# Kernel tuning notes

Measured on AMD Instinct MI355X. Metric: run time of the kernel, lower is better.

The kernel has to match this reference:

```python
import jax, jax.numpy as jnp
import numpy as np
from jax import lax

B, S, N, FD = 4, 12, 307, 3
E = 64; F = 64; H = 64; K = 3; HEADS = 4; P = 12; DFF = 64


def setup_inputs() -> dict:
    key = jax.random.key(0)
    ks = jax.random.split(key, 24)
    rn = lambda i, shape, s=0.1: jax.random.normal(ks[i], shape, dtype=jnp.float32) * s
    z = lambda n: jnp.zeros((n,), jnp.float32)
    return {
        'x': jax.random.normal(ks[0], (B, S, N, FD), dtype=jnp.float32),
        'cheb': rn(1, (K, N, N), 0.05),
        'theta': rn(2, (K, E, F)),
        'W_emb_x': rn(3, (1, E)), 'b_emb_x': z(E),
        'W_emb_os': rn(4, (FD - 1, E)), 'b_emb_os': z(E),
        'U_x': rn(5, (F, 4 * H)), 'V_x': rn(6, (H, 4 * H)), 'b_x': z(4 * H),
        'U_g': rn(7, (F, 2 * H)), 'V_g': rn(8, (H, 2 * H)), 'b_g': z(2 * H),
        'W_ff1': rn(9, (H, DFF)), 'b_ff1': z(DFF), 'W_ff2': rn(10, (DFF, H)), 'b_ff2': z(H),
        'W_tc': rn(11, (F, H, 1, 3)), 'b_tc': z(F),
        'W_rc': rn(12, (F, H, 1, 1)), 'b_rc': z(F),
        'W_in': rn(13, (3 * F, F)), 'b_in': z(3 * F),
        'W_out': rn(14, (F, F)), 'b_out': z(F),
        'W_fa1': rn(15, (F, DFF)), 'b_fa1': z(DFF), 'W_fa2': rn(16, (DFF, F)), 'b_fa2': z(F),
        'W_fin': rn(17, (P, S, 1, F)), 'b_fin': z(P),
    }


def _forward(x, cheb, theta, W_emb_x, b_emb_x, W_emb_os, b_emb_os,
             U_x, V_x, b_x, U_g, V_g, b_g, W_ff1, b_ff1, W_ff2, b_ff2,
             W_tc, b_tc, W_rc, b_rc, W_in, b_in, W_out, b_out,
             W_fa1, b_fa1, W_fa2, b_fa2, W_fin, b_fin):
    # token embeddings (dropout=0 -> identity)
    emb_x = x[..., :1] @ W_emb_x + b_emb_x          # (B,S,N,E)
    emb_os = x[..., 1:] @ W_emb_os + b_emb_os       # (B,S,N,E)

    def cheb_conv(h):
        # sum_k relu-after-sum of T_k @ h @ theta_k
        agg = jnp.einsum('kmn,bsnc->kbsmc', cheb, h)
        return jax.nn.relu(jnp.einsum('kbsmc,kcd->bsmd', agg, theta))

    gcn_x = cheb_conv(emb_x)                        # (B,S,N,F)
    gcn_os = cheb_conv(emb_os)                      # (B,S,N,F)

    # Glstm: precompute input projections, scan the recurrence over time
    gx = jnp.einsum('bsnc,cf->sbnf', gcn_x, U_x) + b_x    # (S,B,N,4H)
    gg = jnp.einsum('bsnc,cf->sbnf', gcn_os, U_g) + b_g   # (S,B,N,2H)

    h0 = jnp.zeros((B, N, H), x.dtype)
    c0 = jnp.zeros((B, N, H), x.dtype)

    def step(carry, inp):
        ht, ct = carry
        gx_t, gg_t = inp
        gates = jax.nn.sigmoid(gx_t + ht @ V_x)     # ft,it,ot,ut all sigmoid (as in source)
        gov = jax.nn.sigmoid(gg_t + ht @ V_g)
        ft, it, ot, ut = jnp.split(gates, 4, axis=-1)
        gf, gu = jnp.split(gov, 2, axis=-1)
        ct = gf * ft * ct + gu * it * ut
        ht = ot * jnp.tanh(ct)
        return (ht, ct), ht

    _, hs = lax.scan(step, (h0, c0), (gx, gg))
    hidden = jnp.moveaxis(hs, 0, 1)                 # (B,S,N,H)
    # Muti_glstm output feedforward
    hidden = jax.nn.relu(hidden @ W_ff1 + b_ff1) @ W_ff2 + b_ff2

    # time conv: (1,3) kernel over time axis, pad 1
    hs_nchw = jnp.transpose(hidden, (0, 3, 2, 1))   # (B,H,N,S)
    tc = lax.conv_general_dilated(hs_nchw, W_tc, (1, 1), ((0, 0), (1, 1)),
                                  dimension_numbers=('NCHW', 'OIHW', 'NCHW'))
    tc = jnp.transpose(tc + b_tc[None, :, None, None], (0, 3, 2, 1))  # (B,S,N,F)

    # query = last time step, repeated over S
    query = jnp.broadcast_to(tc[:, -1:], (B, S, N, F))
    q_in = jnp.reshape(jnp.swapaxes(query, 2, 3), (B * N, S, F))
    kv_in = jnp.reshape(jnp.swapaxes(emb_x, 2, 3), (B * N, S, E))

    # torch MHA (batch_first=False): seq axis is dim0 (L=B*N), batch axis is dim1 (S)
    hd = F // HEADS
    Wq, Wk, Wv = jnp.split(W_in, 3, axis=0)
    bq, bk, bv = jnp.split(b_in, 3)

    def proj(t, Wp, bp):
        L = t.shape[0]
        p = t @ Wp.T + bp                            # (L, S, F)
        return jnp.transpose(p.reshape(L, S * HEADS, hd), (1, 0, 2))  # (S*HEADS, L, hd)

    qh = proj(q_in, Wq, bq)
    kh = proj(kv_in, Wk, bk)
    vh = proj(kv_in, Wv, bv)
    scores = jnp.einsum('hld,hmd->hlm', qh, kh) / np.float32(np.sqrt(hd))
    attn = jax.nn.softmax(scores, axis=-1)
    ctx = jnp.einsum('hlm,hmd->hld', attn, vh)       # (S*HEADS, B*N, hd)
    ctx = jnp.transpose(ctx, (1, 0, 2)).reshape(B * N, S, F)
    dsa = ctx @ W_out.T + b_out                      # (B*N, S, F)

    dsa = jnp.swapaxes(dsa.reshape(B, N, S, F), 1, 2)  # (B,S,N,F)
    ffa = jax.nn.relu(dsa @ W_fa1 + b_fa1) @ W_fa2 + b_fa2
    # residual 1x1 conv over channels of hidden
    res = jnp.einsum('bsnh,fh->bsnf', hidden, W_rc[:, :, 0, 0]) + b_rc
    comb = res + ffa                                 # (B,S,N,F)
    # final conv: channels=S, kernel (1,F) valid, then take last width index
    out = jnp.einsum('bsnf,psf->bpn', comb, W_fin[:, :, 0, :]) + b_fin[None, :, None]
    return out                                       # (B, pre_len, N)


def reference(x, cheb, theta, W_emb_x, b_emb_x, W_emb_os, b_emb_os,
              U_x, V_x, b_x, U_g, V_g, b_g, W_ff1, b_ff1, W_ff2, b_ff2,
              W_tc, b_tc, W_rc, b_rc, W_in, b_in, W_out, b_out,
              W_fa1, b_fa1, W_fa2, b_fa2, W_fin, b_fin):
    return _forward(x, cheb, theta, W_emb_x, b_emb_x, W_emb_os, b_emb_os,
                    U_x, V_x, b_x, U_g, V_g, b_g, W_ff1, b_ff1, W_ff2, b_ff2,
                    W_tc, b_tc, W_rc, b_rc, W_in, b_in, W_out, b_out,
                    W_fa1, b_fa1, W_fa2, b_fa2, W_fin, b_fin)
```

## Files before the change

kernel.cpp:

```cpp
#include <hip/hip_runtime.h>
#include <hip/hip_bf16.h>

#define BB 4
#define SS 12
#define NN 307
#define LL 1228
#define BSC 48
#define GG 48
#define WS_CX    0
#define WS_CROW  132624
#define WS_TXD   133568
#define WS_TBD   133760
#define WS_T1D   133952
#define WS_T2D   134144
#define WS_TOB   134336
#define WS_WRCT  134528
#define WS_WOT   138624
#define WS_H2    142720
#define WS_TFL   1085824
#define WS_XFL   1164416
#define WS_QH    2107520
#define WS_KH    3050624
#define WS_VH    3993728
#define WS_CTX   4936832

__global__ __launch_bounds__(256) void k1_precomp(
    const float* __restrict__ theta, const float* __restrict__ Wex,
    const float* __restrict__ bex, const float* __restrict__ Weos,
    const float* __restrict__ beos, const float* __restrict__ W_rc,
    const float* __restrict__ W_out, float* __restrict__ ws) {
  int tid = threadIdx.x;
  if (tid < 192) {
    int k = tid / 64, d = tid % 64;
    float a0 = 0.f, a1 = 0.f, a2 = 0.f, a3 = 0.f, a4 = 0.f;
    for (int c = 0; c < 64; ++c) {
      float th = theta[(k * 64 + c) * 64 + d];
      a0 = fmaf(Wex[c], th, a0);
      a1 = fmaf(bex[c], th, a1);
      a2 = fmaf(Weos[c], th, a2);
      a3 = fmaf(Weos[64 + c], th, a3);
      a4 = fmaf(beos[c], th, a4);
    }
    ws[WS_TXD + tid] = a0; ws[WS_TBD + tid] = a1; ws[WS_T1D + tid] = a2;
    ws[WS_T2D + tid] = a3; ws[WS_TOB + tid] = a4;
  }
  for (int i = tid; i < 4096; i += 256) {
    int hh = i >> 6, f = i & 63;
    ws[WS_WRCT + i] = W_rc[f * 64 + hh];
    ws[WS_WOT + i]  = W_out[f * 64 + hh];
  }
}

__global__ __launch_bounds__(320) void k2_cx(const float* __restrict__ x,
                                             const float* __restrict__ cheb,
                                             float* __restrict__ ws) {
  int k = blockIdx.x / BSC, bs = blockIdx.x % BSC;
  __shared__ float xl[921];
  for (int i = threadIdx.x; i < 921; i += 320) xl[i] = x[bs * 921 + i];
  __syncthreads();
  int m = threadIdx.x;
  if (m < NN) {
    const float* ch = cheb + (k * NN + m) * NN;
    float a0 = 0.f, a1 = 0.f, a2 = 0.f, ar = 0.f;
    for (int n = 0; n < NN; ++n) {
      float c = ch[n];
      ar += c;
      a0 = fmaf(c, xl[3 * n], a0);
      a1 = fmaf(c, xl[3 * n + 1], a1);
      a2 = fmaf(c, xl[3 * n + 2], a2);
    }
    ws[WS_CX + ((k * 3 + 0) * BSC + bs) * NN + m] = a0;
    ws[WS_CX + ((k * 3 + 1) * BSC + bs) * NN + m] = a1;
    ws[WS_CX + ((k * 3 + 2) * BSC + bs) * NN + m] = a2;
    if (bs == 0) ws[WS_CROW + k * NN + m] = ar;
  }
}

__global__ __launch_bounds__(256) void k2c_xfl(const float* __restrict__ x,
                                               const float* __restrict__ Wex,
                                               const float* __restrict__ bex,
                                               float* __restrict__ ws) {
  int idx = blockIdx.x * 256 + threadIdx.x;
  if (idx < 943104) {
    int n = idx % NN;
    int t = idx / NN;
    int e = t & 63;
    int bs = t >> 6;
    ws[WS_XFL + idx] = fmaf(x[(bs * NN + n) * 3], Wex[e], bex[e]);
  }
}

__global__ __launch_bounds__(384) void k3_scan(
    const float* __restrict__ U_x, const float* __restrict__ V_x,
    const float* __restrict__ b_x, const float* __restrict__ U_g,
    const float* __restrict__ V_g, const float* __restrict__ b_g,
    const float* __restrict__ W_ff1, const float* __restrict__ b_ff1,
    const float* __restrict__ W_ff2, const float* __restrict__ b_ff2,
    const float* __restrict__ W_tc, const float* __restrict__ b_tc,
    float* __restrict__ ws) {
  int l = blockIdx.x;
  int b = l / NN, n = l % NN;
  int tid = threadIdx.x;
  __shared__ float gcx[768], gcos[768], hsb[768], sg[256], sv[128];

  for (int idx = tid; idx < 768; idx += 384) {
    int s = idx >> 6, d = idx & 63;
    int bs = b * SS + s;
    float ax = 0.f, ao = 0.f;
#pragma unroll
    for (int k = 0; k < 3; ++k) {
      float c0 = ws[WS_CX + ((k * 3 + 0) * BSC + bs) * NN + n];
      float c1 = ws[WS_CX + ((k * 3 + 1) * BSC + bs) * NN + n];
      float c2 = ws[WS_CX + ((k * 3 + 2) * BSC + bs) * NN + n];
      float cr = ws[WS_CROW + k * NN + n];
      ax += c0 * ws[WS_TXD + k * 64 + d] + cr * ws[WS_TBD + k * 64 + d];
      ao += c1 * ws[WS_T1D + k * 64 + d] + c2 * ws[WS_T2D + k * 64 + d] +
            cr * ws[WS_TOB + k * 64 + d];
    }
    gcx[idx] = fmaxf(ax, 0.f);
    gcos[idx] = fmaxf(ao, 0.f);
  }
  __syncthreads();

  float gr[12];
  float vcol[64];
  if (tid < 256) {
#pragma unroll
    for (int s = 0; s < 12; ++s) gr[s] = b_x[tid];
    for (int c = 0; c < 64; ++c) {
      float u = U_x[c * 256 + tid];
#pragma unroll
      for (int s = 0; s < 12; ++s) gr[s] = fmaf(gcx[s * 64 + c], u, gr[s]);
    }
#pragma unroll
    for (int c = 0; c < 64; ++c) vcol[c] = V_x[c * 256 + tid];
  } else {
    int j = tid - 256;
#pragma unroll
    for (int s = 0; s < 12; ++s) gr[s] = b_g[j];
    for (int c = 0; c < 64; ++c) {
      float u = U_g[c * 128 + j];
#pragma unroll
      for (int s = 0; s < 12; ++s) gr[s] = fmaf(gcos[s * 64 + c], u, gr[s]);
    }
#pragma unroll
    for (int c = 0; c < 64; ++c) vcol[c] = V_g[c * 128 + j];
  }

  float ct = 0.f;
  for (int s = 0; s < 12; ++s) {
    float a = gr[s];
    if (s > 0) {
      const float* hp = &hsb[(s - 1) * 64];
#pragma unroll
      for (int h = 0; h < 64; ++h) a = fmaf(hp[h], vcol[h], a);
    }
    float sig = 1.f / (1.f + __expf(-a));
    if (tid < 256) sg[tid] = sig; else sv[tid - 256] = sig;
    __syncthreads();
    if (tid < 64) {
      ct = sv[tid] * sg[tid] * ct + sv[64 + tid] * sg[64 + tid] * sg[192 + tid];
      hsb[s * 64 + tid] = sg[128 + tid] * tanhf(ct);
    }
    __syncthreads();
  }

  for (int idx = tid; idx < 768; idx += 384) {
    int s = idx >> 6, d = idx & 63;
    float a = b_ff1[d];
    for (int c = 0; c < 64; ++c) a = fmaf(hsb[s * 64 + c], W_ff1[c * 64 + d], a);
    gcx[idx] = fmaxf(a, 0.f);
  }
  __syncthreads();
  for (int idx = tid; idx < 768; idx += 384) {
    int s = idx >> 6, h = idx & 63;
    float a = b_ff2[h];
    for (int d = 0; d < 64; ++d) a = fmaf(gcx[s * 64 + d], W_ff2[d * 64 + h], a);
    ws[WS_H2 + ((b * SS + s) * NN + n) * 64 + h] = a;
    gcos[idx] = a;
  }
  __syncthreads();
  if (tid < 64) {
    int f = tid;
    float a = b_tc[f];
    for (int h = 0; h < 64; ++h) {
      a = fmaf(gcos[10 * 64 + h], W_tc[(f * 64 + h) * 3 + 0], a);
      a = fmaf(gcos[11 * 64 + h], W_tc[(f * 64 + h) * 3 + 1], a);
    }
    ws[WS_TFL + (b * 64 + f) * NN + n] = a;
  }
}

__global__ __launch_bounds__(256) void k5_qkv(const float* __restrict__ W_in,
                                              const float* __restrict__ b_in,
                                              float* __restrict__ ws) {
  int blk = blockIdx.x;
  int g = blk / 77, mt = blk % 77;
  int s = g >> 2, a = g & 3;
  int m0 = mt * 16;
  __shared__ float xw[16][64], qw[16][64];
  for (int i = threadIdx.x; i < 1024; i += 256) {
    int mi = i >> 6, e = i & 63;
    int m = m0 + mi;
    if (m < LL) {
      int base = m * 768 + s * 64;
      xw[mi][e] = ws[WS_XFL + base + e];
      int bq = base / 235776;
      int off = base % 19648;
      qw[mi][e] = ws[WS_TFL + bq * 19648 + off + e];
    }
  }
  __syncthreads();
  int mi = threadIdx.x >> 4, d = threadIdx.x & 15;
  int m = m0 + mi;
  if (m < LL) {
    int f = a * 16 + d;
    float aq = b_in[f], ak = b_in[64 + f], av = b_in[128 + f];
    for (int e = 0; e < 64; ++e) {
      aq = fmaf(qw[mi][e], W_in[f * 64 + e], aq);
      ak = fmaf(xw[mi][e], W_in[(64 + f) * 64 + e], ak);
      av = fmaf(xw[mi][e], W_in[(128 + f) * 64 + e], av);
    }
    int o = (g * LL + m) * 16 + d;
    ws[WS_QH + o] = aq; ws[WS_KH + o] = ak; ws[WS_VH + o] = av;
  }
}

__global__ __launch_bounds__(512) void k6_attn(float* __restrict__ ws) {
  int blk = blockIdx.x;
  int g = blk / 20, qt = blk % 20;
  int s = g >> 2, a = g & 3;
  int tid = threadIdx.x;
  int w = tid >> 6;
  int qi = tid & 63;
  int l = qt * 64 + qi;
  bool act = (l < LL);

  __shared__ float sh[9728];
  float* kt = sh;
  float* vt = sh + 4096;

  float q[16];
  if (act) {
    const float4* qp = reinterpret_cast<const float4*>(ws + WS_QH + (g * LL + l) * 16);
#pragma unroll
    for (int jj = 0; jj < 4; ++jj) {
      float4 t = qp[jj];
      q[4 * jj + 0] = t.x * 0.25f; q[4 * jj + 1] = t.y * 0.25f;
      q[4 * jj + 2] = t.z * 0.25f; q[4 * jj + 3] = t.w * 0.25f;
    }
  } else {
#pragma unroll
    for (int d = 0; d < 16; ++d) q[d] = 0.f;
  }
  float cx[16];
#pragma unroll
  for (int d = 0; d < 16; ++d) cx[d] = 0.f;
  float mx = -1e30f, den = 0.f;

  const float4* kb = reinterpret_cast<const float4*>(ws + WS_KH + g * LL * 16);
  const float4* vb = reinterpret_cast<const float4*>(ws + WS_VH + g * LL * 16);
  float4* kt4 = reinterpret_cast<float4*>(kt);
  float4* vt4 = reinterpret_cast<float4*>(vt);

  for (int mt = 0; mt < 5; ++mt) {
    int mbase = mt * 256;
    int cnt = LL - mbase; if (cnt > 256) cnt = 256;
    int nf4 = cnt * 4;
    for (int i = tid; i < nf4; i += 512) {
      kt4[i] = kb[mbase * 4 + i];
      vt4[i] = vb[mbase * 4 + i];
    }
    __syncthreads();
    int e0 = w * 32;
    int e1 = e0 + 32; if (e1 > cnt) e1 = cnt;
    for (int mi = e0; mi < e1; ++mi) {
      const float4* kp = kt4 + mi * 4;
      float4 ka = kp[0], kb4 = kp[1], kc = kp[2], kd = kp[3];
      float p = q[0] * ka.x;
      p = fmaf(q[1], ka.y, p);  p = fmaf(q[2], ka.z, p);  p = fmaf(q[3], ka.w, p);
      p = fmaf(q[4], kb4.x, p); p = fmaf(q[5], kb4.y, p); p = fmaf(q[6], kb4.z, p);
      p = fmaf(q[7], kb4.w, p); p = fmaf(q[8], kc.x, p);  p = fmaf(q[9], kc.y, p);
      p = fmaf(q[10], kc.z, p); p = fmaf(q[11], kc.w, p); p = fmaf(q[12], kd.x, p);
      p = fmaf(q[13], kd.y, p); p = fmaf(q[14], kd.z, p); p = fmaf(q[15], kd.w, p);
      if (p > mx) {
        float r = __expf(mx - p);
        den *= r;
#pragma unroll
        for (int d = 0; d < 16; ++d) cx[d] *= r;
        mx = p;
      }
      float wgt = __expf(p - mx);
      den += wgt;
      const float4* vp = vt4 + mi * 4;
      float4 va = vp[0], vb4 = vp[1], vc = vp[2], vd = vp[3];
      cx[0]  = fmaf(wgt, va.x, cx[0]);  cx[1]  = fmaf(wgt, va.y, cx[1]);
      cx[2]  = fmaf(wgt, va.z, cx[2]);  cx[3]  = fmaf(wgt, va.w, cx[3]);
      cx[4]  = fmaf(wgt, vb4.x, cx[4]); cx[5]  = fmaf(wgt, vb4.y, cx[5]);
      cx[6]  = fmaf(wgt, vb4.z, cx[6]); cx[7]  = fmaf(wgt, vb4.w, cx[7]);
      cx[8]  = fmaf(wgt, vc.x, cx[8]);  cx[9]  = fmaf(wgt, vc.y, cx[9]);
      cx[10] = fmaf(wgt, vc.z, cx[10]); cx[11] = fmaf(wgt, vc.w, cx[11]);
      cx[12] = fmaf(wgt, vd.x, cx[12]); cx[13] = fmaf(wgt, vd.y, cx[13]);
      cx[14] = fmaf(wgt, vd.z, cx[14]); cx[15] = fmaf(wgt, vd.w, cx[15]);
    }
    __syncthreads();
  }

  float* smx  = sh;
  float* sden = sh + 512;
  float* scx  = sh + 1024;
  smx[w * 64 + qi] = mx;
  sden[w * 64 + qi] = den;
#pragma unroll
  for (int d = 0; d < 16; ++d) scx[(w * 64 + qi) * 17 + d] = cx[d];
  __syncthreads();

  if (tid < 256) {
    int q2 = tid >> 2, jj = tid & 3;
    int l2 = qt * 64 + q2;
    if (l2 < LL) {
      float m = smx[q2];
#pragma unroll
      for (int u = 1; u < 8; ++u) m = fmaxf(m, smx[u * 64 + q2]);
      float dtot = 0.f;
      float c0 = 0.f, c1 = 0.f, c2 = 0.f, c3 = 0.f;
#pragma unroll
      for (int u = 0; u < 8; ++u) {
        float r = __expf(smx[u * 64 + q2] - m);
        dtot = fmaf(sden[u * 64 + q2], r, dtot);
        const float* cp = &scx[(u * 64 + q2) * 17 + jj * 4];
        c0 = fmaf(cp[0], r, c0); c1 = fmaf(cp[1], r, c1);
        c2 = fmaf(cp[2], r, c2); c3 = fmaf(cp[3], r, c3);
      }
      float inv = 1.f / dtot;
      float* op = ws + WS_CTX + (l2 * SS + s) * 64 + a * 16 + jj * 4;
      *reinterpret_cast<float4*>(op) =
          make_float4(c0 * inv, c1 * inv, c2 * inv, c3 * inv);
    }
  }
}

__global__ __launch_bounds__(64) void k7_out(
    const float* __restrict__ W_fa1, const float* __restrict__ b_fa1,
    const float* __restrict__ W_fa2, const float* __restrict__ b_fa2,
    const float* __restrict__ b_rc, const float* __restrict__ b_out,
    const float* __restrict__ W_fin, const float* __restrict__ b_fin,
    const float* __restrict__ ws, float* __restrict__ out) {
  int l = blockIdx.x, b = l / NN, n = l % NN;
  int f = threadIdx.x;
  __shared__ float h2r[64], ctr[64], dsr[64], tr[64], comb[768];
  for (int s = 0; s < 12; ++s) {
    h2r[f] = ws[WS_H2 + ((b * SS + s) * NN + n) * 64 + f];
    ctr[f] = ws[WS_CTX + (l * SS + s) * 64 + f];
    __syncthreads();
    float a = b_out[f];
    for (int q = 0; q < 64; ++q) a = fmaf(ctr[q], ws[WS_WOT + q * 64 + f], a);
    dsr[f] = a;
    __syncthreads();
    float t = b_fa1[f];
    for (int q = 0; q < 64; ++q) t = fmaf(dsr[q], W_fa1[q * 64 + f], t);
    tr[f] = fmaxf(t, 0.f);
    float r = b_rc[f];
    for (int q = 0; q < 64; ++q) r = fmaf(h2r[q], ws[WS_WRCT + q * 64 + f], r);
    __syncthreads();
    float ff = b_fa2[f];
    for (int q = 0; q < 64; ++q) ff = fmaf(tr[q], W_fa2[q * 64 + f], ff);
    comb[s * 64 + f] = r + ff;
    __syncthreads();
  }
  if (f < 12) {
    float o = b_fin[f];
    for (int i = 0; i < 768; ++i) {
      int s = i >> 6, q = i & 63;
      o = fmaf(comb[i], W_fin[(f * SS + s) * 64 + q], o);
    }
    out[(b * SS + f) * NN + n] = o;
  }
}

extern "C" void kernel_launch(void* const* d_in, const int* in_sizes, int n_in,
                              void* d_out, int out_size, void* d_ws, size_t ws_size,
                              hipStream_t stream) {
  (void)in_sizes; (void)n_in; (void)out_size; (void)ws_size;
  const float* x     = (const float*)d_in[0];
  const float* cheb  = (const float*)d_in[1];
  const float* theta = (const float*)d_in[2];
  const float* Wex   = (const float*)d_in[3];
  const float* bex   = (const float*)d_in[4];
  const float* Weos  = (const float*)d_in[5];
  const float* beos  = (const float*)d_in[6];
  const float* U_x   = (const float*)d_in[7];
  const float* V_x   = (const float*)d_in[8];
  const float* b_x   = (const float*)d_in[9];
  const float* U_g   = (const float*)d_in[10];
  const float* V_g   = (const float*)d_in[11];
  const float* b_g   = (const float*)d_in[12];
  const float* W_ff1 = (const float*)d_in[13];
  const float* b_ff1 = (const float*)d_in[14];
  const float* W_ff2 = (const float*)d_in[15];
  const float* b_ff2 = (const float*)d_in[16];
  const float* W_tc  = (const float*)d_in[17];
  const float* b_tc  = (const float*)d_in[18];
  const float* W_rc  = (const float*)d_in[19];
  const float* b_rc  = (const float*)d_in[20];
  const float* W_in  = (const float*)d_in[21];
  const float* b_in  = (const float*)d_in[22];
  const float* W_out = (const float*)d_in[23];
  const float* b_out = (const float*)d_in[24];
  const float* W_fa1 = (const float*)d_in[25];
  const float* b_fa1 = (const float*)d_in[26];
  const float* W_fa2 = (const float*)d_in[27];
  const float* b_fa2 = (const float*)d_in[28];
  const float* W_fin = (const float*)d_in[29];
  const float* b_fin = (const float*)d_in[30];
  float* ws = (float*)d_ws;
  float* outp = (float*)d_out;

  k1_precomp<<<1, 256, 0, stream>>>(theta, Wex, bex, Weos, beos, W_rc, W_out, ws);
  k2_cx<<<144, 320, 0, stream>>>(x, cheb, ws);
  k2c_xfl<<<3684, 256, 0, stream>>>(x, Wex, bex, ws);
  k3_scan<<<1228, 384, 0, stream>>>(U_x, V_x, b_x, U_g, V_g, b_g,
                                    W_ff1, b_ff1, W_ff2, b_ff2, W_tc, b_tc, ws);
  k5_qkv<<<48 * 77, 256, 0, stream>>>(W_in, b_in, ws);
  k6_attn<<<960, 512, 0, stream>>>(ws);
  k7_out<<<1228, 64, 0, stream>>>(W_fa1, b_fa1, W_fa2, b_fa2, b_rc, b_out,
                                  W_fin, b_fin, ws, outp);
}
```

Baseline: 410.9 us.

## Parallelize output kernel across time steps with 768-thread blocks and wave reduction

The output head kernel now assigns one 64-thread wavefront per time step, so all 12 steps of the out-projection, FFN and residual conv run in parallel instead of looping serially with four barriers per step. The final projection over time and channels becomes a per-wavefront partial sum with a shuffle reduction, replacing a 768-iteration loop run on only 12 threads. Shared memory per block grows and blocks become much larger, which may reduce the number of blocks resident at once.

```diff
diff --git a/kernel.cpp b/kernel.cpp
--- a/kernel.cpp
+++ b/kernel.cpp
@@ -340,42 +340,56 @@
   }
 }
 
-__global__ __launch_bounds__(64) void k7_out(
+__global__ __launch_bounds__(768) void k7_out(
     const float* __restrict__ W_fa1, const float* __restrict__ b_fa1,
     const float* __restrict__ W_fa2, const float* __restrict__ b_fa2,
     const float* __restrict__ b_rc, const float* __restrict__ b_out,
     const float* __restrict__ W_fin, const float* __restrict__ b_fin,
     const float* __restrict__ ws, float* __restrict__ out) {
   int l = blockIdx.x, b = l / NN, n = l % NN;
-  int f = threadIdx.x;
-  __shared__ float h2r[64], ctr[64], dsr[64], tr[64], comb[768];
-  for (int s = 0; s < 12; ++s) {
-    h2r[f] = ws[WS_H2 + ((b * SS + s) * NN + n) * 64 + f];
-    ctr[f] = ws[WS_CTX + (l * SS + s) * 64 + f];
-    __syncthreads();
-    float a = b_out[f];
-    for (int q = 0; q < 64; ++q) a = fmaf(ctr[q], ws[WS_WOT + q * 64 + f], a);
-    dsr[f] = a;
-    __syncthreads();
-    float t = b_fa1[f];
-    for (int q = 0; q < 64; ++q) t = fmaf(dsr[q], W_fa1[q * 64 + f], t);
-    tr[f] = fmaxf(t, 0.f);
-    float r = b_rc[f];
-    for (int q = 0; q < 64; ++q) r = fmaf(h2r[q], ws[WS_WRCT + q * 64 + f], r);
-    __syncthreads();
-    float ff = b_fa2[f];
-    for (int q = 0; q < 64; ++q) ff = fmaf(tr[q], W_fa2[q * 64 + f], ff);
-    comb[s * 64 + f] = r + ff;
-    __syncthreads();
-  }
-  if (f < 12) {
-    float o = b_fin[f];
-    for (int i = 0; i < 768; ++i) {
-      int s = i >> 6, q = i & 63;
-      o = fmaf(comb[i], W_fin[(f * SS + s) * 64 + q], o);
-    }
-    out[(b * SS + f) * NN + n] = o;
-  }
+  int tid = threadIdx.x;
+  int s = tid >> 6, f = tid & 63;
+  __shared__ float ctrL[768], h2rL[768], dsrL[768], trL[768], combL[768];
+
+  ctrL[tid] = ws[WS_CTX + l * 768 + tid];
+  h2rL[tid] = ws[WS_H2 + ((b * SS + s) * NN + n) * 64 + f];
+  __syncthreads();
+
+  float dsr = b_out[f], res = b_rc[f];
+  {
+    const float* cr = &ctrL[s * 64];
+    const float* hr = &h2rL[s * 64];
+    for (int q = 0; q < 64; ++q) {
+      dsr = fmaf(cr[q], ws[WS_WOT + q * 64 + f], dsr);
+      res = fmaf(hr[q], ws[WS_WRCT + q * 64 + f], res);
+    }
+  }
+  dsrL[tid] = dsr;
+  __syncthreads();
+
+  float t = b_fa1[f];
+  {
+    const float* dr = &dsrL[s * 64];
+    for (int q = 0; q < 64; ++q) t = fmaf(dr[q], W_fa1[q * 64 + f], t);
+  }
+  trL[tid] = fmaxf(t, 0.f);
+  __syncthreads();
+
+  float ff = b_fa2[f];
+  {
+    const float* tr2 = &trL[s * 64];
+    for (int q = 0; q < 64; ++q) ff = fmaf(tr2[q], W_fa2[q * 64 + f], ff);
+  }
+  combL[tid] = res + ff;
+  __syncthreads();
+
+  float part = 0.f;
+#pragma unroll
+  for (int k = 0; k < 12; ++k)
+    part = fmaf(combL[k * 64 + f], W_fin[(s * SS + k) * 64 + f], part);
+#pragma unroll
+  for (int off = 32; off; off >>= 1) part += __shfl_down(part, off, 64);
+  if (f == 0) out[(b * SS + s) * NN + n] = part + b_fin[s];
 }
 
 extern "C" void kernel_launch(void* const* d_in, const int* in_sizes, int n_in,
@@ -423,6 +437,6 @@
                                     W_ff1, b_ff1, W_ff2, b_ff2, W_tc, b_tc, ws);
   k5_qkv<<<48 * 77, 256, 0, stream>>>(W_in, b_in, ws);
   k6_attn<<<960, 512, 0, stream>>>(ws);
-  k7_out<<<1228, 64, 0, stream>>>(W_fa1, b_fa1, W_fa2, b_fa2, b_rc, b_out,
-                                  W_fin, b_fin, ws, outp);
-}
+  k7_out<<<1228, 768, 0, stream>>>(W_fa1, b_fa1, W_fa2, b_fa2, b_rc, b_out,
+                                   W_fin, b_fin, ws, outp);
+}
```

Result: slower. 451.0 us (+9.7%).

## Split output stage into per-(l,s) comb kernel and separate final projection kernel

Applied to the files above, without the earlier changes.

The final output kernel previously looped serially over 12 time steps inside one 64-thread block per node. It is now split into a kernel with one block per (node, timestep) that computes the combined residual and feed-forward features into workspace. A second kernel then applies the final conv projection with the weights staged in shared memory. The goal is more parallelism and no serial time loop, at the cost of an extra launch and a round trip through global memory for the combined tensor, which reuses the XFL workspace slot.

```diff
diff --git a/kernel.cpp b/kernel.cpp
--- a/kernel.cpp
+++ b/kernel.cpp
@@ -340,41 +340,59 @@
   }
 }
 
-__global__ __launch_bounds__(64) void k7_out(
+__global__ __launch_bounds__(64) void k7a_comb(
     const float* __restrict__ W_fa1, const float* __restrict__ b_fa1,
     const float* __restrict__ W_fa2, const float* __restrict__ b_fa2,
     const float* __restrict__ b_rc, const float* __restrict__ b_out,
+    float* __restrict__ ws) {
+  int blk = blockIdx.x;
+  int l = blk / SS, s = blk % SS;
+  int b = l / NN, n = l % NN;
+  int f = threadIdx.x;
+  __shared__ float h2r[64], ctr[64], dsrL[64], trL[64];
+
+  h2r[f] = ws[WS_H2 + ((b * SS + s) * NN + n) * 64 + f];
+  ctr[f] = ws[WS_CTX + (l * SS + s) * 64 + f];
+  __syncthreads();
+
+  float dsr = b_out[f], res = b_rc[f];
+  for (int q = 0; q < 64; ++q) {
+    dsr = fmaf(ctr[q], ws[WS_WOT + q * 64 + f], dsr);
+    res = fmaf(h2r[q], ws[WS_WRCT + q * 64 + f], res);
+  }
+  dsrL[f] = dsr;
+  __syncthreads();
+
+  float t = b_fa1[f];
+  for (int q = 0; q < 64; ++q) t = fmaf(dsrL[q], W_fa1[q * 64 + f], t);
+  trL[f] = fmaxf(t, 0.f);
+  __syncthreads();
+
+  float ff = b_fa2[f];
+  for (int q = 0; q < 64; ++q) ff = fmaf(trL[q], W_fa2[q * 64 + f], ff);
+  ws[WS_XFL + (l * SS + s) * 64 + f] = res + ff;
+}
+
+__global__ __launch_bounds__(320) void k7b_fin(
     const float* __restrict__ W_fin, const float* __restrict__ b_fin,
     const float* __restrict__ ws, float* __restrict__ out) {
-  int l = blockIdx.x, b = l / NN, n = l % NN;
-  int f = threadIdx.x;
-  __shared__ float h2r[64], ctr[64], dsr[64], tr[64], comb[768];
-  for (int s = 0; s < 12; ++s) {
-    h2r[f] = ws[WS_H2 + ((b * SS + s) * NN + n) * 64 + f];
-    ctr[f] = ws[WS_CTX + (l * SS + s) * 64 + f];
-    __syncthreads();
-    float a = b_out[f];
-    for (int q = 0; q < 64; ++q) a = fmaf(ctr[q], ws[WS_WOT + q * 64 + f], a);
-    dsr[f] = a;
-    __syncthreads();
-    float t = b_fa1[f];
-    for (int q = 0; q < 64; ++q) t = fmaf(dsr[q], W_fa1[q * 64 + f], t);
-    tr[f] = fmaxf(t, 0.f);
-    float r = b_rc[f];
-    for (int q = 0; q < 64; ++q) r = fmaf(h2r[q], ws[WS_WRCT + q * 64 + f], r);
-    __syncthreads();
-    float ff = b_fa2[f];
-    for (int q = 0; q < 64; ++q) ff = fmaf(tr[q], W_fa2[q * 64 + f], ff);
-    comb[s * 64 + f] = r + ff;
-    __syncthreads();
-  }
-  if (f < 12) {
-    float o = b_fin[f];
-    for (int i = 0; i < 768; ++i) {
-      int s = i >> 6, q = i & 63;
-      o = fmaf(comb[i], W_fin[(f * SS + s) * 64 + q], o);
-    }
-    out[(b * SS + f) * NN + n] = o;
+  int blk = blockIdx.x;
+  int b = blk / SS, p = blk % SS;
+  int tid = threadIdx.x;
+  __shared__ float wf[768];
+  for (int i = tid; i < 768; i += 320) wf[i] = W_fin[p * 768 + i];
+  __syncthreads();
+  int n = tid;
+  if (n < NN) {
+    const float* cb = ws + WS_XFL + (b * NN + n) * 768;
+    float a0 = 0.f, a1 = 0.f, a2 = 0.f, a3 = 0.f;
+    for (int i = 0; i < 768; i += 4) {
+      a0 = fmaf(cb[i], wf[i], a0);
+      a1 = fmaf(cb[i + 1], wf[i + 1], a1);
+      a2 = fmaf(cb[i + 2], wf[i + 2], a2);
+      a3 = fmaf(cb[i + 3], wf[i + 3], a3);
+    }
+    out[(b * SS + p) * NN + n] = (a0 + a1) + (a2 + a3) + b_fin[p];
   }
 }
 
@@ -423,6 +441,7 @@
                                     W_ff1, b_ff1, W_ff2, b_ff2, W_tc, b_tc, ws);
   k5_qkv<<<48 * 77, 256, 0, stream>>>(W_in, b_in, ws);
   k6_attn<<<960, 512, 0, stream>>>(ws);
-  k7_out<<<1228, 64, 0, stream>>>(W_fa1, b_fa1, W_fa2, b_fa2, b_rc, b_out,
-                                  W_fin, b_fin, ws, outp);
-}
+  k7a_comb<<<LL * SS, 64, 0, stream>>>(W_fa1, b_fa1, W_fa2, b_fa2,
+                                       b_rc, b_out, ws);
+  k7b_fin<<<BB * SS, 320, 0, stream>>>(W_fin, b_fin, ws, outp);
+}
```

After: 385.3 us. 1.07x faster.
